# Kernel optimization log

Hardware: AMD Instinct MI355X
Metric: run time of the kernel (lower is better)

## Reference

```python
import jax, jax.numpy as jnp
import numpy as np

IGNORE_INDEX = -100


def setup_inputs() -> dict:
    key = jax.random.key(0)
    k1, k2, k3 = jax.random.split(key, 3)
    N, H, V = 4096, 2048, 50257
    x = jax.random.normal(k1, (N, H), dtype=jnp.float32)
    weight = jax.random.normal(k2, (V, H), dtype=jnp.float32) * (1.0 / np.sqrt(H))
    y = jax.random.randint(k3, (N,), 0, V, dtype=jnp.int64)
    return {"x": x, "weight": weight, "y": y}


def reference(x, weight, y):
    # Fused linear + cross entropy: logits = x @ W^T, mean NLL over non-ignored tokens.
    logits = jnp.einsum("nh,vh->nv", x, weight)  # [N, V]
    logp = jax.nn.log_softmax(logits, axis=-1)
    mask = (y != IGNORE_INDEX)
    safe_y = jnp.where(mask, y, 0)
    nll = -jnp.take_along_axis(logp, safe_y[:, None], axis=-1)[:, 0]  # [N]
    n_valid = jnp.maximum(jnp.sum(mask), 1)
    loss = jnp.sum(jnp.where(mask, nll, 0.0)) / n_valid.astype(nll.dtype)
    return loss
```

## Files before the change

### kernel.cpp

```cpp
#include <hip/hip_runtime.h>
#include <hip/hip_bf16.h>
#include <math.h>

typedef unsigned char  u8;
typedef unsigned int   u32;
typedef __attribute__((ext_vector_type(8)))  int   int8v;
typedef __attribute__((ext_vector_type(16))) float f32x16;

#define IGNORE_INDEX (-100)

__device__ __forceinline__ u8 f32_to_e4m3(float f) {
    union { float f; u32 u; } v; v.f = f;
    u32 s  = (v.u >> 24) & 0x80u;
    u32 au = v.u & 0x7FFFFFFFu;
    float a = __uint_as_float(au);
    if (a >= 448.0f) return (u8)(s | 0x7E);
    int e = (int)(au >> 23) - 127;
    if (e >= -6) {
        u32 m    = au & 0x7FFFFFu;
        u32 keep = m >> 20;
        u32 rest = m & 0xFFFFFu;
        keep += (rest > 0x80000u) || (rest == 0x80000u && (keep & 1u));
        u32 code = ((u32)(e + 7) << 3) + keep;
        if (code > 0x7E) code = 0x7E;
        return (u8)(s | code);
    } else {
        int q = (int)rintf(a * 512.0f);
        return (u8)(s | (u32)q);
    }
}

__global__ __launch_bounds__(256) void cvt_pack_fp8(const float* __restrict__ in,
                                                    u8* __restrict__ out,
                                                    float scale, int H, int nRows) {
    __shared__ __align__(16) u8 lds[16384];
    const int kc    = blockIdx.x;
    const int panel = blockIdx.y;
    const int t     = threadIdx.x;

#pragma unroll
    for (int it = 0; it < 4; ++it) {
        int u  = it * 256 + t;
        int r  = u >> 3;
        int cc = u & 7;
        int row = panel * 128 + r;
        u8 tmp[16];
        if (row < nRows) {
            const float* src = in + (size_t)row * H + kc * 128 + cc * 16;
#pragma unroll
            for (int p = 0; p < 4; ++p) {
                float4 f = *(const float4*)(src + p * 4);
                tmp[p * 4 + 0] = f32_to_e4m3(f.x * scale);
                tmp[p * 4 + 1] = f32_to_e4m3(f.y * scale);
                tmp[p * 4 + 2] = f32_to_e4m3(f.z * scale);
                tmp[p * 4 + 3] = f32_to_e4m3(f.w * scale);
            }
        } else {
#pragma unroll
            for (int p = 0; p < 16; ++p) tmp[p] = 0;
        }
        int i2 = r >> 5, ln32 = r & 31;
        int ks = cc >> 2, khalf = (cc >> 1) & 1, h = cc & 1;
        int s  = i2 * 4 + ks * 2 + h;
        int lane = khalf * 32 + ln32;
        *(int4*)(lds + s * 1024 + lane * 16) = *(const int4*)tmp;
    }
    __syncthreads();

    u8* dst = out + ((size_t)panel * gridDim.x + kc) * 16384;
    const int4* l4 = (const int4*)lds;
    int4* d4 = (int4*)dst;
#pragma unroll
    for (int p = 0; p < 4; ++p)
        d4[p * 256 + t] = l4[p * 256 + t];
}

#define LD8(dst, base, off) { \
    int4 lo_ = *(const int4*)((base) + (off)); \
    int4 hi_ = *(const int4*)((base) + (off) + 1024); \
    dst[0]=lo_.x; dst[1]=lo_.y; dst[2]=lo_.z; dst[3]=lo_.w; \
    dst[4]=hi_.x; dst[5]=hi_.y; dst[6]=hi_.z; dst[7]=hi_.w; }

__global__ __launch_bounds__(256) void gemm_lse_partial(
    const u8* __restrict__ Ap,
    const u8* __restrict__ Bp,
    float2* __restrict__ partials,
    int KC, int V, int VT)
{
    __shared__ float2 red[256];

    const int tid  = threadIdx.x;
    const int w    = tid >> 6;
    const int lane = tid & 63;
    const int wm   = w >> 1, wn = w & 1;
    const int ln32 = lane & 31;
    const int khalf = lane >> 5;

    const int mBase = blockIdx.x * 128;
    const int vTile = blockIdx.y;
    const int vBase = vTile * 128;

    f32x16 acc[2][2];
#pragma unroll
    for (int i = 0; i < 2; ++i)
#pragma unroll
        for (int j = 0; j < 2; ++j)
#pragma unroll
            for (int r = 0; r < 16; ++r) acc[i][j][r] = 0.0f;

    const int scaleA = 0x7C7C7C7C;
    const int scaleB = 0x7B7B7B7B;

    const u8* aPtr = Ap + ((size_t)blockIdx.x * KC) * 16384 + lane * 16;
    const u8* bPtr = Bp + ((size_t)vTile      * KC) * 16384 + lane * 16;

    const int aO0 = (wm * 2    ) * 4096;
    const int aO1 = (wm * 2 + 1) * 4096;
    const int bO0 = (wn * 2    ) * 4096;
    const int bO1 = (wn * 2 + 1) * 4096;

#pragma unroll 2
    for (int kc = 0; kc < KC; ++kc) {
        int8v a00, a10, b00, b10, a01, a11, b01, b11;
        LD8(a00, aPtr, aO0);           LD8(a10, aPtr, aO1);
        LD8(b00, bPtr, bO0);           LD8(b10, bPtr, bO1);
        LD8(a01, aPtr, aO0 + 2048);    LD8(a11, aPtr, aO1 + 2048);
        LD8(b01, bPtr, bO0 + 2048);    LD8(b11, bPtr, bO1 + 2048);

        acc[0][0] = __builtin_amdgcn_mfma_scale_f32_32x32x64_f8f6f4(a00, b00, acc[0][0], 0, 0, 0, scaleA, 0, scaleB);
        acc[0][1] = __builtin_amdgcn_mfma_scale_f32_32x32x64_f8f6f4(a00, b10, acc[0][1], 0, 0, 0, scaleA, 0, scaleB);
        acc[1][0] = __builtin_amdgcn_mfma_scale_f32_32x32x64_f8f6f4(a10, b00, acc[1][0], 0, 0, 0, scaleA, 0, scaleB);
        acc[1][1] = __builtin_amdgcn_mfma_scale_f32_32x32x64_f8f6f4(a10, b10, acc[1][1], 0, 0, 0, scaleA, 0, scaleB);
        acc[0][0] = __builtin_amdgcn_mfma_scale_f32_32x32x64_f8f6f4(a01, b01, acc[0][0], 0, 0, 0, scaleA, 0, scaleB);
        acc[0][1] = __builtin_amdgcn_mfma_scale_f32_32x32x64_f8f6f4(a01, b11, acc[0][1], 0, 0, 0, scaleA, 0, scaleB);
        acc[1][0] = __builtin_amdgcn_mfma_scale_f32_32x32x64_f8f6f4(a11, b01, acc[1][0], 0, 0, 0, scaleA, 0, scaleB);
        acc[1][1] = __builtin_amdgcn_mfma_scale_f32_32x32x64_f8f6f4(a11, b11, acc[1][1], 0, 0, 0, scaleA, 0, scaleB);

        aPtr += 16384; bPtr += 16384;
    }

    bool vj[2];
#pragma unroll
    for (int j = 0; j < 2; ++j)
        vj[j] = (vBase + wn * 64 + j * 32 + ln32) < V;

#pragma unroll
    for (int i = 0; i < 2; ++i) {
#pragma unroll
        for (int r = 0; r < 16; ++r) {
            float v0 = vj[0] ? acc[i][0][r] : -INFINITY;
            float v1 = vj[1] ? acc[i][1][r] : -INFINITY;
            float m = fmaxf(v0, v1);
#pragma unroll
            for (int o = 1; o < 32; o <<= 1)
                m = fmaxf(m, __shfl_xor(m, o, 64));
            float s = 0.0f;
            if (vj[0]) s += __expf(acc[i][0][r] - m);
            if (vj[1]) s += __expf(acc[i][1][r] - m);
#pragma unroll
            for (int o = 1; o < 32; o <<= 1)
                s += __shfl_xor(s, o, 64);
            if (ln32 == 0) {
                int row = wm * 64 + i * 32 + (r & 3) + 8 * (r >> 2) + 4 * khalf;
                red[row * 2 + wn] = make_float2(m, s);
            }
        }
    }
    __syncthreads();

    if (tid < 128) {
        float2 p0 = red[tid * 2 + 0];
        float2 p1 = red[tid * 2 + 1];
        float m = fmaxf(p0.x, p1.x);
        float s = p0.y * __expf(p0.x - m) + p1.y * __expf(p1.x - m);
        partials[(size_t)(mBase + tid) * VT + vTile] = make_float2(m, s);
    }
}

__global__ __launch_bounds__(256) void row_final(
    const float* __restrict__ x,
    const float* __restrict__ W,
    const int* __restrict__ y,
    const float2* __restrict__ partials,
    float* __restrict__ nll, float* __restrict__ valid,
    int H, int V, int VT)
{
    const int n = blockIdx.x;
    const int t = threadIdx.x;
    const int yn = y[n];
    const bool ok = (yn != IGNORE_INDEX);

    float dsum = 0.0f;
    if (ok) {
        int cy = yn; if (cy < 0) cy = 0; if (cy >= V) cy = V - 1;
        const float4* xr = (const float4*)(x + (size_t)n * H);
        const float4* wr = (const float4*)(W + (size_t)cy * H);
        int nf4 = H >> 2;
        for (int i = t; i < nf4; i += 256) {
            float4 a = xr[i], b = wr[i];
            dsum += a.x * b.x + a.y * b.y + a.z * b.z + a.w * b.w;
        }
    }

    float m = -INFINITY, s = 0.0f;
    const float2* pr = partials + (size_t)n * VT;
    for (int i = t; i < VT; i += 256) {
        float2 p = pr[i];
        float nm = fmaxf(m, p.x);
        s = s * __expf(m - nm) + p.y * __expf(p.x - nm);
        m = nm;
    }

    __shared__ float rm[256], rs[256], rd[256];
    rm[t] = m; rs[t] = s; rd[t] = dsum;
    __syncthreads();
    for (int o = 128; o > 0; o >>= 1) {
        if (t < o) {
            float m2 = rm[t + o], s2 = rs[t + o];
            float nm = fmaxf(rm[t], m2);
            rs[t] = rs[t] * __expf(rm[t] - nm) + s2 * __expf(m2 - nm);
            rm[t] = nm;
            rd[t] += rd[t + o];
        }
        __syncthreads();
    }
    if (t == 0) {
        float lse = rm[0] + __logf(rs[0]);
        nll[n]   = ok ? (lse - rd[0]) : 0.0f;
        valid[n] = ok ? 1.0f : 0.0f;
    }
}

__global__ __launch_bounds__(1024) void final_loss(
    const float* __restrict__ nll, const float* __restrict__ valid,
    float* __restrict__ out, int n)
{
    __shared__ float ss[1024], sv[1024];
    const int t = threadIdx.x;
    float a = 0.0f, b = 0.0f;
    for (int i = t; i < n; i += 1024) { a += nll[i]; b += valid[i]; }
    ss[t] = a; sv[t] = b;
    __syncthreads();
    for (int o = 512; o > 0; o >>= 1) {
        if (t < o) { ss[t] += ss[t + o]; sv[t] += sv[t + o]; }
        __syncthreads();
    }
    if (t == 0) out[0] = ss[0] / fmaxf(sv[0], 1.0f);
}

extern "C" void kernel_launch(void* const* d_in, const int* in_sizes, int n_in,
                              void* d_out, int out_size, void* d_ws, size_t ws_size,
                              hipStream_t stream) {
    const float* x = (const float*)d_in[0];
    const float* W = (const float*)d_in[1];
    const int*   y = (const int*)d_in[2];

    const long xsz = in_sizes[0];
    const long wsz = in_sizes[1];
    const int  N   = in_sizes[2];
    const int  H   = (int)(xsz / N);
    const int  V   = (int)(wsz / H);
    const int  VT  = (V + 127) / 128;
    const int  MT  = N / 128;
    const int  KC  = H / 128;

    char* ws = (char*)d_ws;
    size_t off = 0;
    u8* Wp = (u8*)(ws + off); off += (size_t)VT * KC * 16384; off = (off + 255) & ~(size_t)255;
    u8* Xp = (u8*)(ws + off); off += (size_t)MT * KC * 16384; off = (off + 255) & ~(size_t)255;
    float2* partials = (float2*)(ws + off); off += (size_t)N * VT * sizeof(float2); off = (off + 255) & ~(size_t)255;
    float* nll   = (float*)(ws + off); off += (size_t)N * 4;
    float* valid = (float*)(ws + off); off += (size_t)N * 4;

    cvt_pack_fp8<<<dim3(KC, VT), 256, 0, stream>>>(W, Wp, 16.0f, H, V);
    cvt_pack_fp8<<<dim3(KC, MT), 256, 0, stream>>>(x, Xp, 8.0f, H, N);

    dim3 grid(MT, VT);
    gemm_lse_partial<<<grid, 256, 0, stream>>>(Xp, Wp, partials, KC, V, VT);

    row_final<<<N, 256, 0, stream>>>(x, W, y, partials, nll, valid, H, V, VT);
    final_loss<<<1, 1024, 0, stream>>>(nll, valid, (float*)d_out, N);
}
```

Measured before the change: 1.205 ms.

## Use 256x256 tiles with triple-buffered LDS staging via global_load_lds

Enlarges the GEMM+LSE tile from 128x128 to 256x256 with 512 threads and 8 waves. Operands are staged into triple-buffered LDS through direct global-to-LDS loads, with manual waitcnt and barriers. A grid swizzle is added for L2 locality, and MFMA issue runs at raised priority. The goal is to cut redundant global/L2 operand traffic (the old kernel read fragments straight from global with no reuse across waves) and to overlap loads with MFMA. In exchange it uses 96KB+ of LDS per block, more registers for 8 accumulators, and adds sync hazards in the hand-written waitcnt logic.

```diff
diff --git a/kernel.cpp b/kernel.cpp
--- a/kernel.cpp
+++ b/kernel.cpp
@@ -75,34 +75,42 @@
         d4[p * 256 + t] = l4[p * 256 + t];
 }
 
-#define LD8(dst, base, off) { \
-    int4 lo_ = *(const int4*)((base) + (off)); \
-    int4 hi_ = *(const int4*)((base) + (off) + 1024); \
-    dst[0]=lo_.x; dst[1]=lo_.y; dst[2]=lo_.z; dst[3]=lo_.w; \
-    dst[4]=hi_.x; dst[5]=hi_.y; dst[6]=hi_.z; dst[7]=hi_.w; }
-
-__global__ __launch_bounds__(256) void gemm_lse_partial(
+__device__ __forceinline__ void gl_lds16(const u8* g, u8* l) {
+    __builtin_amdgcn_global_load_lds(
+        (const __attribute__((address_space(1))) void*)g,
+        (__attribute__((address_space(3))) void*)l, 16, 0, 0);
+}
+
+__global__ __launch_bounds__(512, 2) void gemm_lse_partial(
     const u8* __restrict__ Ap,
     const u8* __restrict__ Bp,
     float2* __restrict__ partials,
-    int KC, int V, int VT)
+    int KC, int V, int VT, int MT)
 {
-    __shared__ float2 red[256];
-
-    const int tid  = threadIdx.x;
-    const int w    = tid >> 6;
-    const int lane = tid & 63;
-    const int wm   = w >> 1, wn = w & 1;
-    const int ln32 = lane & 31;
+    __shared__ __align__(16) u8 sA3[3][16384];
+    __shared__ __align__(16) u8 sB3[3][16384];
+    __shared__ float2 red[256 * 4];
+
+    const int tid   = threadIdx.x;
+    const int w     = tid >> 6;
+    const int lane  = tid & 63;
+    const int wm    = w >> 2;
+    const int wn    = w & 3;
+    const int ln32  = lane & 31;
     const int khalf = lane >> 5;
-
-    const int mBase = blockIdx.x * 128;
-    const int vTile = blockIdx.y;
-    const int vBase = vTile * 128;
-
-    f32x16 acc[2][2];
-#pragma unroll
-    for (int i = 0; i < 2; ++i)
+    const int l16   = lane * 16;
+
+    const int nwg = MT * VT;
+    int orig = blockIdx.x;
+    int swz  = orig;
+    if ((nwg & 7) == 0) { int cpx = nwg >> 3; swz = (orig & 7) * cpx + (orig >> 3); }
+    const int bx = swz % MT;
+    const int by = swz / MT;
+    const int bx2 = bx * 2, by2 = by * 2;
+
+    f32x16 acc[4][2];
+#pragma unroll
+    for (int i = 0; i < 4; ++i)
 #pragma unroll
         for (int j = 0; j < 2; ++j)
 #pragma unroll
@@ -111,70 +119,100 @@
     const int scaleA = 0x7C7C7C7C;
     const int scaleB = 0x7B7B7B7B;
 
-    const u8* aPtr = Ap + ((size_t)blockIdx.x * KC) * 16384 + lane * 16;
-    const u8* bPtr = Bp + ((size_t)vTile      * KC) * 16384 + lane * 16;
-
-    const int aO0 = (wm * 2    ) * 4096;
-    const int aO1 = (wm * 2 + 1) * 4096;
-    const int bO0 = (wn * 2    ) * 4096;
-    const int bO1 = (wn * 2 + 1) * 4096;
-
-#pragma unroll 2
-    for (int kc = 0; kc < KC; ++kc) {
-        int8v a00, a10, b00, b10, a01, a11, b01, b11;
-        LD8(a00, aPtr, aO0);           LD8(a10, aPtr, aO1);
-        LD8(b00, bPtr, bO0);           LD8(b10, bPtr, bO1);
-        LD8(a01, aPtr, aO0 + 2048);    LD8(a11, aPtr, aO1 + 2048);
-        LD8(b01, bPtr, bO0 + 2048);    LD8(b11, bPtr, bO1 + 2048);
-
-        acc[0][0] = __builtin_amdgcn_mfma_scale_f32_32x32x64_f8f6f4(a00, b00, acc[0][0], 0, 0, 0, scaleA, 0, scaleB);
-        acc[0][1] = __builtin_amdgcn_mfma_scale_f32_32x32x64_f8f6f4(a00, b10, acc[0][1], 0, 0, 0, scaleA, 0, scaleB);
-        acc[1][0] = __builtin_amdgcn_mfma_scale_f32_32x32x64_f8f6f4(a10, b00, acc[1][0], 0, 0, 0, scaleA, 0, scaleB);
-        acc[1][1] = __builtin_amdgcn_mfma_scale_f32_32x32x64_f8f6f4(a10, b10, acc[1][1], 0, 0, 0, scaleA, 0, scaleB);
-        acc[0][0] = __builtin_amdgcn_mfma_scale_f32_32x32x64_f8f6f4(a01, b01, acc[0][0], 0, 0, 0, scaleA, 0, scaleB);
-        acc[0][1] = __builtin_amdgcn_mfma_scale_f32_32x32x64_f8f6f4(a01, b11, acc[0][1], 0, 0, 0, scaleA, 0, scaleB);
-        acc[1][0] = __builtin_amdgcn_mfma_scale_f32_32x32x64_f8f6f4(a11, b01, acc[1][0], 0, 0, 0, scaleA, 0, scaleB);
-        acc[1][1] = __builtin_amdgcn_mfma_scale_f32_32x32x64_f8f6f4(a11, b11, acc[1][1], 0, 0, 0, scaleA, 0, scaleB);
-
-        aPtr += 16384; bPtr += 16384;
-    }
-
-    bool vj[2];
-#pragma unroll
-    for (int j = 0; j < 2; ++j)
-        vj[j] = (vBase + wn * 64 + j * 32 + ln32) < V;
-
-#pragma unroll
-    for (int i = 0; i < 2; ++i) {
+#define MFMA(av, bv, c) __builtin_amdgcn_mfma_scale_f32_32x32x64_f8f6f4(av, bv, c, 0, 0, 0, scaleA, 0, scaleB)
+
+#define STAGE(T_, B_) do { \
+    int kc_ = (T_) >> 1, ks_ = (T_) & 1; \
+    for (int k_ = 0; k_ < 2; ++k_) { \
+        int cA_  = w * 2 + k_; \
+        int pnl_ = cA_ >> 3, sub_ = cA_ & 7; \
+        int s_   = (sub_ >> 1) * 4 + ks_ * 2 + (sub_ & 1); \
+        gl_lds16(Ap + ((size_t)(bx2 + pnl_) * KC + kc_) * 16384 + s_ * 1024 + l16, \
+                 &sA3[B_][cA_ * 1024]); \
+        gl_lds16(Bp + ((size_t)(by2 + pnl_) * KC + kc_) * 16384 + s_ * 1024 + l16, \
+                 &sB3[B_][cA_ * 1024]); \
+    } } while (0)
+
+#define LDF(dst, base, off) do { \
+    int4 lo_ = *(const int4*)((base) + (off) + l16); \
+    int4 hi_ = *(const int4*)((base) + (off) + 1024 + l16); \
+    dst[0]=lo_.x; dst[1]=lo_.y; dst[2]=lo_.z; dst[3]=lo_.w; \
+    dst[4]=hi_.x; dst[5]=hi_.y; dst[6]=hi_.z; dst[7]=hi_.w; } while (0)
+
+    const int aOff = wm * 8192;
+    const int bOff = (wn >> 1) * 8192 + (wn & 1) * 4096;
+
+    const int T = KC * 2;
+    STAGE(0, 0);
+    STAGE(1, 1);
+    asm volatile("s_waitcnt vmcnt(4)\n\ts_barrier" ::: "memory");
+
+    int cur = 0;
+#pragma unroll 1
+    for (int t = 0; t < T; ++t) {
+        const u8* bA = &sA3[cur][0];
+        const u8* bB = &sB3[cur][0];
+        int8v a0, a1, a2, a3, b0v, b1v;
+        LDF(a0, bA, aOff);           LDF(a1, bA, aOff + 2048);
+        LDF(a2, bA, aOff + 4096);    LDF(a3, bA, aOff + 6144);
+        LDF(b0v, bB, bOff);          LDF(b1v, bB, bOff + 2048);
+
+        int nb = cur + 2; if (nb >= 3) nb -= 3;
+        if (t + 2 < T) STAGE(t + 2, nb);
+
+        __builtin_amdgcn_s_setprio(1);
+        acc[0][0] = MFMA(a0, b0v, acc[0][0]); acc[0][1] = MFMA(a0, b1v, acc[0][1]);
+        acc[1][0] = MFMA(a1, b0v, acc[1][0]); acc[1][1] = MFMA(a1, b1v, acc[1][1]);
+        acc[2][0] = MFMA(a2, b0v, acc[2][0]); acc[2][1] = MFMA(a2, b1v, acc[2][1]);
+        acc[3][0] = MFMA(a3, b0v, acc[3][0]); acc[3][1] = MFMA(a3, b1v, acc[3][1]);
+        __builtin_amdgcn_s_setprio(0);
+
+        if (t + 2 < T) asm volatile("s_waitcnt vmcnt(4) lgkmcnt(0)\n\ts_barrier" ::: "memory");
+        else           asm volatile("s_waitcnt vmcnt(0) lgkmcnt(0)\n\ts_barrier" ::: "memory");
+        cur = cur + 1; if (cur >= 3) cur -= 3;
+    }
+
+    bool vj0 = (by * 256 + wn * 64 + ln32)      < V;
+    bool vj1 = (by * 256 + wn * 64 + 32 + ln32) < V;
+
+#pragma unroll
+    for (int i2 = 0; i2 < 4; ++i2) {
 #pragma unroll
         for (int r = 0; r < 16; ++r) {
-            float v0 = vj[0] ? acc[i][0][r] : -INFINITY;
-            float v1 = vj[1] ? acc[i][1][r] : -INFINITY;
-            float m = fmaxf(v0, v1);
+            float x0 = vj0 ? acc[i2][0][r] : -INFINITY;
+            float x1 = vj1 ? acc[i2][1][r] : -INFINITY;
+            float m = fmaxf(x0, x1);
 #pragma unroll
             for (int o = 1; o < 32; o <<= 1)
                 m = fmaxf(m, __shfl_xor(m, o, 64));
             float s = 0.0f;
-            if (vj[0]) s += __expf(acc[i][0][r] - m);
-            if (vj[1]) s += __expf(acc[i][1][r] - m);
+            if (vj0) s += __expf(acc[i2][0][r] - m);
+            if (vj1) s += __expf(acc[i2][1][r] - m);
 #pragma unroll
             for (int o = 1; o < 32; o <<= 1)
                 s += __shfl_xor(s, o, 64);
             if (ln32 == 0) {
-                int row = wm * 64 + i * 32 + (r & 3) + 8 * (r >> 2) + 4 * khalf;
-                red[row * 2 + wn] = make_float2(m, s);
+                int row = wm * 128 + i2 * 32 + (r & 3) + 8 * (r >> 2) + 4 * khalf;
+                red[row * 4 + wn] = make_float2(m, s);
             }
         }
     }
     __syncthreads();
 
-    if (tid < 128) {
-        float2 p0 = red[tid * 2 + 0];
-        float2 p1 = red[tid * 2 + 1];
-        float m = fmaxf(p0.x, p1.x);
-        float s = p0.y * __expf(p0.x - m) + p1.y * __expf(p1.x - m);
-        partials[(size_t)(mBase + tid) * VT + vTile] = make_float2(m, s);
-    }
+    if (tid < 256) {
+        float m = -INFINITY, s = 0.0f;
+#pragma unroll
+        for (int q = 0; q < 4; ++q) {
+            float2 p = red[tid * 4 + q];
+            float nm = fmaxf(m, p.x);
+            s = s * __expf(m - nm) + p.y * __expf(p.x - nm);
+            m = nm;
+        }
+        partials[(size_t)(bx * 256 + tid) * VT + by] = make_float2(m, s);
+    }
+#undef MFMA
+#undef STAGE
+#undef LDF
 }
 
 __global__ __launch_bounds__(256) void row_final(
@@ -260,23 +298,24 @@
     const int  N   = in_sizes[2];
     const int  H   = (int)(xsz / N);
     const int  V   = (int)(wsz / H);
-    const int  VT  = (V + 127) / 128;
-    const int  MT  = N / 128;
+    const int  VT  = (V + 255) / 256;
+    const int  PV  = VT * 2;
+    const int  MT  = N / 256;
+    const int  PM  = N / 128;
     const int  KC  = H / 128;
 
     char* ws = (char*)d_ws;
     size_t off = 0;
-    u8* Wp = (u8*)(ws + off); off += (size_t)VT * KC * 16384; off = (off + 255) & ~(size_t)255;
-    u8* Xp = (u8*)(ws + off); off += (size_t)MT * KC * 16384; off = (off + 255) & ~(size_t)255;
+    u8* Wp = (u8*)(ws + off); off += (size_t)PV * KC * 16384; off = (off + 255) & ~(size_t)255;
+    u8* Xp = (u8*)(ws + off); off += (size_t)PM * KC * 16384; off = (off + 255) & ~(size_t)255;
     float2* partials = (float2*)(ws + off); off += (size_t)N * VT * sizeof(float2); off = (off + 255) & ~(size_t)255;
     float* nll   = (float*)(ws + off); off += (size_t)N * 4;
     float* valid = (float*)(ws + off); off += (size_t)N * 4;
 
-    cvt_pack_fp8<<<dim3(KC, VT), 256, 0, stream>>>(W, Wp, 16.0f, H, V);
-    cvt_pack_fp8<<<dim3(KC, MT), 256, 0, stream>>>(x, Xp, 8.0f, H, N);
-
-    dim3 grid(MT, VT);
-    gemm_lse_partial<<<grid, 256, 0, stream>>>(Xp, Wp, partials, KC, V, VT);
+    cvt_pack_fp8<<<dim3(KC, PV), 256, 0, stream>>>(W, Wp, 16.0f, H, V);
+    cvt_pack_fp8<<<dim3(KC, PM), 256, 0, stream>>>(x, Xp, 8.0f, H, N);
+
+    gemm_lse_partial<<<dim3(MT * VT), dim3(512), 0, stream>>>(Xp, Wp, partials, KC, V, VT, MT);
 
     row_final<<<N, 256, 0, stream>>>(x, W, y, partials, nll, valid, H, V, VT);
     final_loss<<<1, 1024, 0, stream>>>(nll, valid, (float*)d_out, N);
```

Result: slower. 1.333 ms (+10.6%).

## Enlarge GEMM tile to 256 rows and use hardware fp8 pack conversion

Applied to the files above, without the earlier changes.

The fused GEMM+LSE kernel now gives each block 256 rows (4 M-subtiles per wave, each wave owning one 128-row panel), which halves the number of M blocks and doubles B reuse per load. Operand loads are split into two K halves to limit live registers, and launch_bounds(256,2) is added. The fp8 conversion kernel uses the hardware cvt_pk_fp8_f32 builtin instead of software rounding. This cuts B traffic and conversion ALU work, but costs more accumulator registers and may reduce occupancy. The hardware conversion may also round slightly differently at saturation.

```diff
diff --git a/kernel.cpp b/kernel.cpp
--- a/kernel.cpp
+++ b/kernel.cpp
@@ -30,6 +30,19 @@
     }
 }
 
+__device__ __forceinline__ u32 cvt4_e4m3(float4 f, float scale) {
+#if __has_builtin(__builtin_amdgcn_cvt_pk_fp8_f32)
+    int pk = 0;
+    pk = __builtin_amdgcn_cvt_pk_fp8_f32(f.x * scale, f.y * scale, pk, false);
+    pk = __builtin_amdgcn_cvt_pk_fp8_f32(f.z * scale, f.w * scale, pk, true);
+    return (u32)pk;
+#else
+    u32 b0 = f32_to_e4m3(f.x * scale), b1 = f32_to_e4m3(f.y * scale);
+    u32 b2 = f32_to_e4m3(f.z * scale), b3 = f32_to_e4m3(f.w * scale);
+    return b0 | (b1 << 8) | (b2 << 16) | (b3 << 24);
+#endif
+}
+
 __global__ __launch_bounds__(256) void cvt_pack_fp8(const float* __restrict__ in,
                                                     u8* __restrict__ out,
                                                     float scale, int H, int nRows) {
@@ -44,20 +57,15 @@
         int r  = u >> 3;
         int cc = u & 7;
         int row = panel * 128 + r;
-        u8 tmp[16];
+        u32 tmp[4];
         if (row < nRows) {
             const float* src = in + (size_t)row * H + kc * 128 + cc * 16;
 #pragma unroll
-            for (int p = 0; p < 4; ++p) {
-                float4 f = *(const float4*)(src + p * 4);
-                tmp[p * 4 + 0] = f32_to_e4m3(f.x * scale);
-                tmp[p * 4 + 1] = f32_to_e4m3(f.y * scale);
-                tmp[p * 4 + 2] = f32_to_e4m3(f.z * scale);
-                tmp[p * 4 + 3] = f32_to_e4m3(f.w * scale);
-            }
+            for (int p = 0; p < 4; ++p)
+                tmp[p] = cvt4_e4m3(*(const float4*)(src + p * 4), scale);
         } else {
 #pragma unroll
-            for (int p = 0; p < 16; ++p) tmp[p] = 0;
+            for (int p = 0; p < 4; ++p) tmp[p] = 0;
         }
         int i2 = r >> 5, ln32 = r & 31;
         int ks = cc >> 2, khalf = (cc >> 1) & 1, h = cc & 1;
@@ -81,13 +89,13 @@
     dst[0]=lo_.x; dst[1]=lo_.y; dst[2]=lo_.z; dst[3]=lo_.w; \
     dst[4]=hi_.x; dst[5]=hi_.y; dst[6]=hi_.z; dst[7]=hi_.w; }
 
-__global__ __launch_bounds__(256) void gemm_lse_partial(
+__global__ __launch_bounds__(256, 2) void gemm_lse_partial(
     const u8* __restrict__ Ap,
     const u8* __restrict__ Bp,
     float2* __restrict__ partials,
     int KC, int V, int VT)
 {
-    __shared__ float2 red[256];
+    __shared__ float2 red[256 * 2];
 
     const int tid  = threadIdx.x;
     const int w    = tid >> 6;
@@ -96,13 +104,14 @@
     const int ln32 = lane & 31;
     const int khalf = lane >> 5;
 
-    const int mBase = blockIdx.x * 128;
-    const int vTile = blockIdx.y;
-    const int vBase = vTile * 128;
-
-    f32x16 acc[2][2];
-#pragma unroll
-    for (int i = 0; i < 2; ++i)
+    const int mBase  = blockIdx.x * 256;
+    const int mPanel = blockIdx.x * 2 + wm;
+    const int vTile  = blockIdx.y;
+    const int vBase  = vTile * 128;
+
+    f32x16 acc[4][2];
+#pragma unroll
+    for (int i = 0; i < 4; ++i)
 #pragma unroll
         for (int j = 0; j < 2; ++j)
 #pragma unroll
@@ -111,70 +120,70 @@
     const int scaleA = 0x7C7C7C7C;
     const int scaleB = 0x7B7B7B7B;
 
-    const u8* aPtr = Ap + ((size_t)blockIdx.x * KC) * 16384 + lane * 16;
-    const u8* bPtr = Bp + ((size_t)vTile      * KC) * 16384 + lane * 16;
-
-    const int aO0 = (wm * 2    ) * 4096;
-    const int aO1 = (wm * 2 + 1) * 4096;
-    const int bO0 = (wn * 2    ) * 4096;
-    const int bO1 = (wn * 2 + 1) * 4096;
+    const u8* aPtr = Ap + ((size_t)mPanel * KC) * 16384 + lane * 16;
+    const u8* bPtr = Bp + ((size_t)vTile  * KC) * 16384 + lane * 16;
+
+    const int b0O = (wn * 2    ) * 4096;
+    const int b1O = (wn * 2 + 1) * 4096;
+
+#define MFMA(av, bv, c) __builtin_amdgcn_mfma_scale_f32_32x32x64_f8f6f4(av, bv, c, 0, 0, 0, scaleA, 0, scaleB)
 
 #pragma unroll 2
     for (int kc = 0; kc < KC; ++kc) {
-        int8v a00, a10, b00, b10, a01, a11, b01, b11;
-        LD8(a00, aPtr, aO0);           LD8(a10, aPtr, aO1);
-        LD8(b00, bPtr, bO0);           LD8(b10, bPtr, bO1);
-        LD8(a01, aPtr, aO0 + 2048);    LD8(a11, aPtr, aO1 + 2048);
-        LD8(b01, bPtr, bO0 + 2048);    LD8(b11, bPtr, bO1 + 2048);
-
-        acc[0][0] = __builtin_amdgcn_mfma_scale_f32_32x32x64_f8f6f4(a00, b00, acc[0][0], 0, 0, 0, scaleA, 0, scaleB);
-        acc[0][1] = __builtin_amdgcn_mfma_scale_f32_32x32x64_f8f6f4(a00, b10, acc[0][1], 0, 0, 0, scaleA, 0, scaleB);
-        acc[1][0] = __builtin_amdgcn_mfma_scale_f32_32x32x64_f8f6f4(a10, b00, acc[1][0], 0, 0, 0, scaleA, 0, scaleB);
-        acc[1][1] = __builtin_amdgcn_mfma_scale_f32_32x32x64_f8f6f4(a10, b10, acc[1][1], 0, 0, 0, scaleA, 0, scaleB);
-        acc[0][0] = __builtin_amdgcn_mfma_scale_f32_32x32x64_f8f6f4(a01, b01, acc[0][0], 0, 0, 0, scaleA, 0, scaleB);
-        acc[0][1] = __builtin_amdgcn_mfma_scale_f32_32x32x64_f8f6f4(a01, b11, acc[0][1], 0, 0, 0, scaleA, 0, scaleB);
-        acc[1][0] = __builtin_amdgcn_mfma_scale_f32_32x32x64_f8f6f4(a11, b01, acc[1][0], 0, 0, 0, scaleA, 0, scaleB);
-        acc[1][1] = __builtin_amdgcn_mfma_scale_f32_32x32x64_f8f6f4(a11, b11, acc[1][1], 0, 0, 0, scaleA, 0, scaleB);
+        int8v a0, a1, a2, a3, b0v, b1v;
+        LD8(a0, aPtr, 0);        LD8(a1, aPtr, 4096);
+        LD8(a2, aPtr, 8192);     LD8(a3, aPtr, 12288);
+        LD8(b0v, bPtr, b0O);     LD8(b1v, bPtr, b1O);
+        acc[0][0] = MFMA(a0, b0v, acc[0][0]); acc[0][1] = MFMA(a0, b1v, acc[0][1]);
+        acc[1][0] = MFMA(a1, b0v, acc[1][0]); acc[1][1] = MFMA(a1, b1v, acc[1][1]);
+        acc[2][0] = MFMA(a2, b0v, acc[2][0]); acc[2][1] = MFMA(a2, b1v, acc[2][1]);
+        acc[3][0] = MFMA(a3, b0v, acc[3][0]); acc[3][1] = MFMA(a3, b1v, acc[3][1]);
+        LD8(a0, aPtr, 2048);         LD8(a1, aPtr, 4096 + 2048);
+        LD8(a2, aPtr, 8192 + 2048);  LD8(a3, aPtr, 12288 + 2048);
+        LD8(b0v, bPtr, b0O + 2048);  LD8(b1v, bPtr, b1O + 2048);
+        acc[0][0] = MFMA(a0, b0v, acc[0][0]); acc[0][1] = MFMA(a0, b1v, acc[0][1]);
+        acc[1][0] = MFMA(a1, b0v, acc[1][0]); acc[1][1] = MFMA(a1, b1v, acc[1][1]);
+        acc[2][0] = MFMA(a2, b0v, acc[2][0]); acc[2][1] = MFMA(a2, b1v, acc[2][1]);
+        acc[3][0] = MFMA(a3, b0v, acc[3][0]); acc[3][1] = MFMA(a3, b1v, acc[3][1]);
 
         aPtr += 16384; bPtr += 16384;
     }
 
-    bool vj[2];
-#pragma unroll
-    for (int j = 0; j < 2; ++j)
-        vj[j] = (vBase + wn * 64 + j * 32 + ln32) < V;
-
-#pragma unroll
-    for (int i = 0; i < 2; ++i) {
+    bool vj0 = (vBase + wn * 64 + ln32)      < V;
+    bool vj1 = (vBase + wn * 64 + 32 + ln32) < V;
+
+#pragma unroll
+    for (int i2 = 0; i2 < 4; ++i2) {
 #pragma unroll
         for (int r = 0; r < 16; ++r) {
-            float v0 = vj[0] ? acc[i][0][r] : -INFINITY;
-            float v1 = vj[1] ? acc[i][1][r] : -INFINITY;
-            float m = fmaxf(v0, v1);
+            float x0 = vj0 ? acc[i2][0][r] : -INFINITY;
+            float x1 = vj1 ? acc[i2][1][r] : -INFINITY;
+            float m = fmaxf(x0, x1);
 #pragma unroll
             for (int o = 1; o < 32; o <<= 1)
                 m = fmaxf(m, __shfl_xor(m, o, 64));
             float s = 0.0f;
-            if (vj[0]) s += __expf(acc[i][0][r] - m);
-            if (vj[1]) s += __expf(acc[i][1][r] - m);
+            if (vj0) s += __expf(acc[i2][0][r] - m);
+            if (vj1) s += __expf(acc[i2][1][r] - m);
 #pragma unroll
             for (int o = 1; o < 32; o <<= 1)
                 s += __shfl_xor(s, o, 64);
             if (ln32 == 0) {
-                int row = wm * 64 + i * 32 + (r & 3) + 8 * (r >> 2) + 4 * khalf;
+                int row = wm * 128 + i2 * 32 + (r & 3) + 8 * (r >> 2) + 4 * khalf;
                 red[row * 2 + wn] = make_float2(m, s);
             }
         }
     }
     __syncthreads();
 
-    if (tid < 128) {
+    {
         float2 p0 = red[tid * 2 + 0];
         float2 p1 = red[tid * 2 + 1];
         float m = fmaxf(p0.x, p1.x);
         float s = p0.y * __expf(p0.x - m) + p1.y * __expf(p1.x - m);
         partials[(size_t)(mBase + tid) * VT + vTile] = make_float2(m, s);
     }
+#undef MFMA
 }
 
 __global__ __launch_bounds__(256) void row_final(
@@ -261,19 +270,20 @@
     const int  H   = (int)(xsz / N);
     const int  V   = (int)(wsz / H);
     const int  VT  = (V + 127) / 128;
-    const int  MT  = N / 128;
+    const int  MT  = N / 256;
+    const int  PM  = N / 128;
     const int  KC  = H / 128;
 
     char* ws = (char*)d_ws;
     size_t off = 0;
     u8* Wp = (u8*)(ws + off); off += (size_t)VT * KC * 16384; off = (off + 255) & ~(size_t)255;
-    u8* Xp = (u8*)(ws + off); off += (size_t)MT * KC * 16384; off = (off + 255) & ~(size_t)255;
+    u8* Xp = (u8*)(ws + off); off += (size_t)PM * KC * 16384; off = (off + 255) & ~(size_t)255;
     float2* partials = (float2*)(ws + off); off += (size_t)N * VT * sizeof(float2); off = (off + 255) & ~(size_t)255;
     float* nll   = (float*)(ws + off); off += (size_t)N * 4;
     float* valid = (float*)(ws + off); off += (size_t)N * 4;
 
     cvt_pack_fp8<<<dim3(KC, VT), 256, 0, stream>>>(W, Wp, 16.0f, H, V);
-    cvt_pack_fp8<<<dim3(KC, MT), 256, 0, stream>>>(x, Xp, 8.0f, H, N);
+    cvt_pack_fp8<<<dim3(KC, PM), 256, 0, stream>>>(x, Xp, 8.0f, H, N);
 
     dim3 grid(MT, VT);
     gemm_lse_partial<<<grid, 256, 0, stream>>>(Xp, Wp, partials, KC, V, VT);
```

Result: slower. 1.285 ms (+6.6%).
